# Kernel tuning notes

Hardware: AMD Instinct MI355X
Metric: run time of the kernel (lower is better)

## Reference

```python
import jax, jax.numpy as jnp
import numpy as np

N_NODES = 10000
N_EDGES = 160000
HID = 256
NBOND = 6
NATOM = 62
NLAYERS = 6


def _lin_init(key, fan_in, fan_out):
    # torch nn.Linear default: U(-1/sqrt(fan_in), 1/sqrt(fan_in))
    kw, kb = jax.random.split(key)
    bound = 1.0 / np.sqrt(fan_in)
    w = jax.random.uniform(kw, (fan_in, fan_out), jnp.float32, -bound, bound)
    b = jax.random.uniform(kb, (fan_out,), jnp.float32, -bound, bound)
    return w, b


def setup_inputs() -> dict:
    key = jax.random.key(0)
    ks = jax.random.split(key, 32)
    atom_features = jax.random.normal(ks[0], (N_NODES, NATOM), jnp.float32)
    edge_index = jax.random.randint(ks[1], (2, N_EDGES), 0, N_NODES, jnp.int64 if jax.config.jax_enable_x64 else jnp.int32)
    edge_features = jax.random.normal(ks[2], (N_EDGES, NBOND), jnp.float32)

    embed_w, embed_b = _lin_init(ks[3], NATOM, HID)

    msg_in = 2 * HID + NBOND  # 518
    mw1, mb1, mw2, mb2 = [], [], [], []
    uw1, ub1, uw2, ub2 = [], [], [], []
    for i in range(NLAYERS):
        k = jax.random.split(ks[4 + i], 4)
        w, b = _lin_init(k[0], msg_in, HID); mw1.append(w); mb1.append(b)
        w, b = _lin_init(k[1], HID, HID); mw2.append(w); mb2.append(b)
        w, b = _lin_init(k[2], 2 * HID, HID); uw1.append(w); ub1.append(b)
        w, b = _lin_init(k[3], HID, HID); uw2.append(w); ub2.append(b)

    r_w1, r_b1 = _lin_init(ks[20], HID, HID)
    r_w2, r_b2 = _lin_init(ks[21], HID, HID // 2)
    r_w3, r_b3 = _lin_init(ks[22], HID // 2, 1)

    return {
        "atom_features": atom_features,
        "edge_index": edge_index,
        "edge_features": edge_features,
        "embed_w": embed_w, "embed_b": embed_b,
        "msg_w1": jnp.stack(mw1), "msg_b1": jnp.stack(mb1),
        "msg_w2": jnp.stack(mw2), "msg_b2": jnp.stack(mb2),
        "upd_w1": jnp.stack(uw1), "upd_b1": jnp.stack(ub1),
        "upd_w2": jnp.stack(uw2), "upd_b2": jnp.stack(ub2),
        "r_w1": r_w1, "r_b1": r_b1,
        "r_w2": r_w2, "r_b2": r_b2,
        "r_w3": r_w3, "r_b3": r_b3,
    }


def _mlp2(x, w1, b1, w2, b2):
    return jnp.maximum(x @ w1 + b1, 0.0) @ w2 + b2


def reference(atom_features, edge_index, edge_features,
              embed_w, embed_b,
              msg_w1, msg_b1, msg_w2, msg_b2,
              upd_w1, upd_b1, upd_w2, upd_b2,
              r_w1, r_b1, r_w2, r_b2, r_w3, r_b3):
    src, dst = edge_index[0], edge_index[1]
    n = atom_features.shape[0]
    x = atom_features @ embed_w + embed_b  # [N, H]
    for l in range(msg_w1.shape[0]):
        # per-edge gather + concat -> message MLP
        msg_in = jnp.concatenate([x[src], x[dst], edge_features], axis=-1)  # [E, 2H+B]
        msgs = _mlp2(msg_in, msg_w1[l], msg_b1[l], msg_w2[l], msg_b2[l])  # [E, H]
        # scatter-add into dst nodes
        agg = jax.ops.segment_sum(msgs, dst, num_segments=n)  # [N, H]
        x = _mlp2(jnp.concatenate([x, agg], axis=-1), upd_w1[l], upd_b1[l], upd_w2[l], upd_b2[l])
    # readout (dropout is identity in eval mode)
    h = jnp.maximum(x @ r_w1 + r_b1, 0.0)
    h = jnp.maximum(h @ r_w2 + r_b2, 0.0)
    out = h @ r_w3 + r_b3  # [N, 1]
    return out.mean(axis=0)  # [1]
```

## Files before the change

kernel.cpp:

```cpp
#include <hip/hip_runtime.h>
#include <hip/hip_bf16.h>
#include <hip/hip_fp16.h>


#define HID 256

typedef _Float16 h8 __attribute__((ext_vector_type(8)));
typedef float f32x4 __attribute__((ext_vector_type(4)));

__device__ __forceinline__ void unpack_h8(const int4& r, float* f) {
    const __half2* h = reinterpret_cast<const __half2*>(&r);
#pragma unroll
    for (int k = 0; k < 4; ++k) {
        float2 t = __half22float2(h[k]);
        f[2 * k] = t.x;
        f[2 * k + 1] = t.y;
    }
}

__device__ __forceinline__ void unpack_h4(const int2& r, float* f) {
    const __half2* h = reinterpret_cast<const __half2*>(&r);
    float2 t0 = __half22float2(h[0]);
    float2 t1 = __half22float2(h[1]);
    f[0] = t0.x; f[1] = t0.y; f[2] = t1.x; f[3] = t1.y;
}

__device__ __forceinline__ void gld16(const void* g, void* l) {
    __builtin_amdgcn_global_load_lds(
        (const __attribute__((address_space(1))) void*)g,
        (__attribute__((address_space(3))) void*)l, 16, 0, 0);
}

__device__ __forceinline__ int swz(int row) { return (row + (row >> 2)) & 3; }


__global__ void hist_act_kernel(const int* __restrict__ dst, int* __restrict__ deg,
                                int E, const float* __restrict__ atom,
                                __half* __restrict__ atomH, int NA) {
    int i = blockIdx.x * blockDim.x + threadIdx.x;
    if (i < E) atomicAdd(&deg[dst[i]], 1);
    if (i < NA) {
        int r = i >> 3, seg = i & 7;
        h8 v;
#pragma unroll
        for (int j = 0; j < 8; ++j) {
            int c = seg * 8 + j;
            v[j] = (_Float16)((c < 62) ? atom[(size_t)r * 62 + c] : 0.f);
        }
        *reinterpret_cast<h8*>(&atomH[(size_t)r * 64 + seg * 8]) = v;
    }
}

__global__ __launch_bounds__(256) void scan_kernel(
    const int* __restrict__ deg, int* __restrict__ offs, float* __restrict__ degf, int n) {
    __shared__ int ws[4];
    const int t = threadIdx.x;
    const int lane = t & 63;
    const int w = t >> 6;
    const int per = (n + 255) / 256;
    const int s = t * per;
    const int e = min(s + per, n);
    int sum = 0;
    for (int i = s; i < e; ++i) sum += deg[i];
    int v = sum;
#pragma unroll
    for (int off = 1; off < 64; off <<= 1) {
        int u = __shfl_up(v, off, 64);
        if (lane >= off) v += u;
    }
    if (lane == 63) ws[w] = v;
    __syncthreads();
    if (t == 0) {
        int c = 0;
#pragma unroll
        for (int i = 0; i < 4; ++i) { int x = ws[i]; ws[i] = c; c += x; }
    }
    __syncthreads();
    int run = ws[w] + v - sum;
    for (int i = s; i < e; ++i) {
        int d = deg[i];
        offs[i] = run;
        degf[i] = (float)d;
        run += d;
    }
    if (e == n) offs[n] = run;
}


struct CDesc {
    const float* src;
    __half* dst;
    int Kreal, Kpad, srcN, tile0, dstStride;
};
struct CTab {
    CDesc d[32];
    int nd;
};

__device__ void convert_body(const CTab& tab, int bid) {
    int idx = 0;
    for (int i = 1; i < tab.nd; ++i)
        if (tab.d[i].tile0 <= bid) idx = i;
    const CDesc d = tab.d[idx];
    const int q = bid - d.tile0;
    const int ntN = d.srcN >> 6;
    const int kb = (q / ntN) * 32;
    const int nb = (q % ntN) * 64;
    const int n = nb + (threadIdx.x & 63);
    const int k0 = kb + (threadIdx.x >> 6) * 8;
    h8 v;
#pragma unroll
    for (int j = 0; j < 8; ++j) {
        int k = k0 + j;
        v[j] = (_Float16)((k < d.Kreal) ? d.src[(size_t)k * d.srcN + n] : 0.f);
    }
    *reinterpret_cast<h8*>(&d.dst[(size_t)n * d.dstStride + k0]) = v;
}

__global__ __launch_bounds__(256) void scatter_conv_kernel(
    const int* __restrict__ src, const int* __restrict__ dst,
    const int* __restrict__ offs, int* __restrict__ cursor,
    int* __restrict__ csr_src, const float* __restrict__ ef,
    __half* __restrict__ ef8, int E, int sblocks, CTab tab) {
    if ((int)blockIdx.x < sblocks) {
        int i = blockIdx.x * blockDim.x + threadIdx.x;
        if (i < E) {
            int d = dst[i];
            int pos = atomicAdd(&cursor[d], 1);
            int idx = offs[d] + pos;
            csr_src[idx] = src[i];
            const float* s6 = ef + (size_t)i * 6;
            unsigned short h[8];
#pragma unroll
            for (int j = 0; j < 6; ++j) h[j] = __half_as_ushort(__float2half_rn(s6[j]));
            h[6] = 0; h[7] = 0;
            int4 pk;
            pk.x = (int)(h[0] | ((unsigned)h[1] << 16));
            pk.y = (int)(h[2] | ((unsigned)h[3] << 16));
            pk.z = (int)(h[4] | ((unsigned)h[5] << 16));
            pk.w = (int)(h[6] | ((unsigned)h[7] << 16));
            *reinterpret_cast<int4*>(ef8 + (size_t)idx * 8) = pk;
        }
    } else {
        convert_body(tab, blockIdx.x - sblocks);
    }
}


struct BDesc { float* out; const float* base; const float* v1; const float* B1;
               const float* v2; const float* B2; };
struct BTab { BDesc d[31]; };


#define ASTR 40

struct FDesc { const float* U2; const __half* Wfb; __half* dst; int stride; };
struct FTab { FDesc d[22]; };

__device__ void fold_tile(unsigned char* ldsraw, const FDesc& dd, int t4) {
    _Float16* Ah = (_Float16*)ldsraw;
    _Float16* Bh = (_Float16*)(ldsraw + 64 * ASTR * 2);
    const int rowBase = (t4 >> 2) * 64;
    const int colBase = (t4 & 3) * 64;

    const int tid = threadIdx.x;
    const int lane = tid & 63;
    const int wave = tid >> 6;
    const int waveM = (wave >> 1) * 32;
    const int waveN = (wave & 1) * 32;
    const int m0 = lane & 15;
    const int quad = lane >> 4;
    const int sr = tid >> 2;
    const int sseg = tid & 3;

    const f32x4 z = {0.f, 0.f, 0.f, 0.f};
    f32x4 acc[2][2] = {{z, z}, {z, z}};

    for (int kb = 0; kb < 256; kb += 32) {
        {
            size_t off = (size_t)(rowBase + sr) * 256 + kb + sseg * 8;
            *reinterpret_cast<int4*>(&Ah[sr * ASTR + sseg * 8]) =
                *reinterpret_cast<const int4*>(&dd.Wfb[off]);
        }
        {
            const float* Bp = dd.U2 + (size_t)(colBase + sr) * 256 + kb + sseg * 8;
            float4 u0 = *reinterpret_cast<const float4*>(Bp);
            float4 u1 = *reinterpret_cast<const float4*>(Bp + 4);
            h8 v;
            v[0] = (_Float16)u0.x; v[1] = (_Float16)u0.y;
            v[2] = (_Float16)u0.z; v[3] = (_Float16)u0.w;
            v[4] = (_Float16)u1.x; v[5] = (_Float16)u1.y;
            v[6] = (_Float16)u1.z; v[7] = (_Float16)u1.w;
            *reinterpret_cast<h8*>(&Bh[sr * ASTR + sseg * 8]) = v;
        }
        __syncthreads();

        const h8 a0 = *reinterpret_cast<const h8*>(&Ah[(waveM + m0) * ASTR + quad * 8]);
        const h8 a1 = *reinterpret_cast<const h8*>(&Ah[(waveM + 16 + m0) * ASTR + quad * 8]);
        const h8 b0 = *reinterpret_cast<const h8*>(&Bh[(waveN + m0) * ASTR + quad * 8]);
        const h8 b1 = *reinterpret_cast<const h8*>(&Bh[(waveN + 16 + m0) * ASTR + quad * 8]);

        acc[0][0] = __builtin_amdgcn_mfma_f32_16x16x32_f16(a0, b0, acc[0][0], 0, 0, 0);
        acc[0][1] = __builtin_amdgcn_mfma_f32_16x16x32_f16(a0, b1, acc[0][1], 0, 0, 0);
        acc[1][0] = __builtin_amdgcn_mfma_f32_16x16x32_f16(a1, b0, acc[1][0], 0, 0, 0);
        acc[1][1] = __builtin_amdgcn_mfma_f32_16x16x32_f16(a1, b1, acc[1][1], 0, 0, 0);

        __syncthreads();
    }

#pragma unroll
    for (int tm = 0; tm < 2; ++tm)
#pragma unroll
        for (int reg = 0; reg < 4; ++reg) {
            int n = rowBase + waveM + tm * 16 + quad * 4 + reg;
#pragma unroll
            for (int tn = 0; tn < 2; ++tn) {
                int k = colBase + waveN + tn * 16 + m0;
                dd.dst[(size_t)n * dd.stride + k] = __float2half_rn(acc[tm][tn][reg]);
            }
        }
}


template <int TN>
__device__ void gemm_tile(
    unsigned char* lds, int bx, int by,
    const __half* __restrict__ A, int lda, const __half* __restrict__ A2,
    const __half* __restrict__ W, int K,
    const float* __restrict__ bias, const float* __restrict__ bias2,
    const float* __restrict__ rowscale,
    __half* __restrict__ C, int M, int Nc, int do_relu) {
    constexpr int BUF = 4096 + TN * 2048;

    const int tid = threadIdx.x;
    const int lane = tid & 63;
    const int wave = tid >> 6;
    const int m0 = lane & 15;
    const int quad = lane >> 4;
    const int waveM = (wave >> 1) * 32;
    const int waveN = (wave & 1) * (TN * 16);
    const int rowBase = bx * 64;
    const int colBase = by * (TN * 32);

    const int sa_r = tid >> 2;
    const int sa_ks = (tid & 3) ^ swz(sa_r);
    const int sa_row = min(rowBase + sa_r, M - 1);
    const int sb_r1 = sa_r + 64;
    const int sb_ks1 = (tid & 3) ^ swz(sb_r1);

    int aoff[2], boff[TN];
#pragma unroll
    for (int tm = 0; tm < 2; ++tm) {
        int r = waveM + tm * 16 + m0;
        aoff[tm] = ((r << 2) + (quad ^ swz(r))) << 4;
    }
#pragma unroll
    for (int tn = 0; tn < TN; ++tn) {
        int r = waveN + tn * 16 + m0;
        boff[tn] = 4096 + (((r << 2) + (quad ^ swz(r))) << 4);
    }

    const f32x4 z = {0.f, 0.f, 0.f, 0.f};
    f32x4 acc[2][TN];
#pragma unroll
    for (int tm = 0; tm < 2; ++tm)
#pragma unroll
        for (int tn = 0; tn < TN; ++tn) acc[tm][tn] = z;

    const __half* ga = A + (size_t)sa_row * lda + sa_ks * 8;
    const __half* ga2 = A2 ? A2 + (size_t)sa_row * lda + sa_ks * 8 : nullptr;
    const __half* gb0 = W + (size_t)(colBase + sa_r) * K + sa_ks * 8;
    const __half* gb1 = W + (size_t)(colBase + sb_r1) * K + sb_ks1 * 8;

    auto issue = [&](int p, int kb) {
        unsigned char* base = lds + p * BUF;
        const __half* as = (A2 && kb >= 256) ? (ga2 + (kb - 256)) : (ga + kb);
        gld16(as, base + wave * 1024);
        gld16(gb0 + kb, base + 4096 + wave * 1024);
        if constexpr (TN == 4) gld16(gb1 + kb, base + 8192 + wave * 1024);
    };

    issue(0, 0);
    int p = 0;
    for (int kb = 0; kb < K; kb += 32) {
        const bool has_next = (kb + 32 < K);
        if (has_next) issue(p ^ 1, kb + 32);
        if (has_next) {
            if constexpr (TN == 4)
                asm volatile("s_waitcnt vmcnt(3)" ::: "memory");
            else
                asm volatile("s_waitcnt vmcnt(2)" ::: "memory");
        } else {
            asm volatile("s_waitcnt vmcnt(0)" ::: "memory");
        }
        asm volatile("s_barrier" ::: "memory");

        const unsigned char* base = lds + p * BUF;
        h8 ah[2], bh[TN];
#pragma unroll
        for (int tm = 0; tm < 2; ++tm)
            ah[tm] = *reinterpret_cast<const h8*>(base + aoff[tm]);
#pragma unroll
        for (int tn = 0; tn < TN; ++tn)
            bh[tn] = *reinterpret_cast<const h8*>(base + boff[tn]);
#pragma unroll
        for (int tm = 0; tm < 2; ++tm)
#pragma unroll
            for (int tn = 0; tn < TN; ++tn)
                acc[tm][tn] = __builtin_amdgcn_mfma_f32_16x16x32_f16(
                    ah[tm], bh[tn], acc[tm][tn], 0, 0, 0);
        asm volatile("s_waitcnt lgkmcnt(0)" ::: "memory");
        asm volatile("s_barrier" ::: "memory");
        p ^= 1;
    }

    float cb[TN], db[TN];
    int col[TN];
#pragma unroll
    for (int tn = 0; tn < TN; ++tn) {
        col[tn] = colBase + waveN + tn * 16 + m0;
        cb[tn] = bias ? bias[col[tn]] : 0.f;
        db[tn] = bias2 ? bias2[col[tn]] : 0.f;
    }
#pragma unroll
    for (int tm = 0; tm < 2; ++tm) {
#pragma unroll
        for (int reg = 0; reg < 4; ++reg) {
            int row = rowBase + waveM + tm * 16 + quad * 4 + reg;
            if (row >= M) continue;
            float rs = rowscale ? rowscale[row] : 0.0f;
#pragma unroll
            for (int tn = 0; tn < TN; ++tn) {
                float v = acc[tm][tn][reg] + cb[tn] + rs * db[tn];
                if (do_relu) v = fmaxf(v, 0.f);
                C[(size_t)row * Nc + col[tn]] = __float2half_rn(v);
            }
        }
    }
}

template <int TN>
__global__ __launch_bounds__(256) void mfma_gemm(
    const __half* __restrict__ A, int lda, const __half* __restrict__ A2,
    const __half* __restrict__ W, int K,
    const float* __restrict__ bias, const float* __restrict__ bias2,
    const float* __restrict__ rowscale,
    __half* __restrict__ C, int M, int Nc, int do_relu) {
    __shared__ __align__(16) unsigned char lds[2 * (4096 + TN * 2048)];
    gemm_tile<TN>(lds, blockIdx.x, blockIdx.y, A, lda, A2, W, K,
                  bias, bias2, rowscale, C, M, Nc, do_relu);
}


__global__ __launch_bounds__(256) void fold_bias_embed_kernel(
    FTab ft, BTab bt, int fblocks, int bblocks,
    const __half* __restrict__ atomH, const __half* __restrict__ w_emb,
    const float* __restrict__ emb_b, __half* __restrict__ outX,
    int M, int mblk) {
    __shared__ __align__(16) unsigned char lds[16384];
    int b = blockIdx.x;
    if (b < fblocks) {
        fold_tile(lds, ft.d[b >> 4], b & 15);
        return;
    }
    b -= fblocks;
    if (b < bblocks) {
        const BDesc d = bt.d[b];
        const int j = threadIdx.x;
        float acc = d.base ? d.base[j] : 0.f;
        if (d.v1)
            for (int k = 0; k < 256; ++k) acc = fmaf(d.v1[k], d.B1[(size_t)k * 256 + j], acc);
        if (d.v2)
            for (int k = 0; k < 256; ++k) acc = fmaf(d.v2[k], d.B2[(size_t)k * 256 + j], acc);
        d.out[j] = acc;
        return;
    }
    b -= bblocks;
    gemm_tile<2>(lds, b % mblk, b / mblk, atomH, 64, nullptr, w_emb, 64,
                 emb_b, nullptr, nullptr, outX, M, HID, 0);
}


__global__ __launch_bounds__(256) void aggregate_kernel(
    const __half* __restrict__ PQ, const __half* __restrict__ ef8,
    const int* __restrict__ offs, const int* __restrict__ csr_src,
    const float* __restrict__ W1c, __half* __restrict__ Hagg, int n) {
    const int wave = threadIdx.x >> 6;
    const int lane = threadIdx.x & 63;
    const int node = blockIdx.x * 4 + wave;
    if (node >= n) return;
    const int ch = lane * 4;

    float wc[6][4];
#pragma unroll
    for (int k = 0; k < 6; ++k) {
        float4 w0 = *reinterpret_cast<const float4*>(W1c + k * HID + ch);
        wc[k][0] = w0.x; wc[k][1] = w0.y; wc[k][2] = w0.z; wc[k][3] = w0.w;
    }
    float qb[4];
    unpack_h4(*reinterpret_cast<const int2*>(PQ + (size_t)node * 512 + 256 + ch), qb);

    float acc[4] = {0.f, 0.f, 0.f, 0.f};

    auto fma_edge = [&](const int2& praw, const int4& eraw) {
        float p[4], e[8];
        unpack_h4(praw, p);
        unpack_h8(eraw, e);
#pragma unroll
        for (int i = 0; i < 4; ++i) {
            float h = p[i] + qb[i];
            h = fmaf(e[0], wc[0][i], h);
            h = fmaf(e[1], wc[1][i], h);
            h = fmaf(e[2], wc[2][i], h);
            h = fmaf(e[3], wc[3][i], h);
            h = fmaf(e[4], wc[4][i], h);
            h = fmaf(e[5], wc[5][i], h);
            acc[i] += fmaxf(h, 0.f);
        }
    };

    const int beg = offs[node];
    const int end = offs[node + 1];
    int j = beg;

    while (j + 6 <= end) {
        int s0 = csr_src[j];
        int s1 = csr_src[j + 1];
        int s2 = csr_src[j + 2];
        int s3 = csr_src[j + 3];
        int s4 = csr_src[j + 4];
        int s5 = csr_src[j + 5];
        int4 e0 = *reinterpret_cast<const int4*>(ef8 + (size_t)j * 8);
        int4 e1 = *reinterpret_cast<const int4*>(ef8 + (size_t)(j + 1) * 8);
        int4 e2 = *reinterpret_cast<const int4*>(ef8 + (size_t)(j + 2) * 8);
        int4 e3 = *reinterpret_cast<const int4*>(ef8 + (size_t)(j + 3) * 8);
        int4 e4 = *reinterpret_cast<const int4*>(ef8 + (size_t)(j + 4) * 8);
        int4 e5 = *reinterpret_cast<const int4*>(ef8 + (size_t)(j + 5) * 8);
        int2 p0 = *reinterpret_cast<const int2*>(PQ + (size_t)s0 * 512 + ch);
        int2 p1 = *reinterpret_cast<const int2*>(PQ + (size_t)s1 * 512 + ch);
        int2 p2 = *reinterpret_cast<const int2*>(PQ + (size_t)s2 * 512 + ch);
        int2 p3 = *reinterpret_cast<const int2*>(PQ + (size_t)s3 * 512 + ch);
        int2 p4 = *reinterpret_cast<const int2*>(PQ + (size_t)s4 * 512 + ch);
        int2 p5 = *reinterpret_cast<const int2*>(PQ + (size_t)s5 * 512 + ch);
        fma_edge(p0, e0);
        fma_edge(p1, e1);
        fma_edge(p2, e2);
        fma_edge(p3, e3);
        fma_edge(p4, e4);
        fma_edge(p5, e5);
        j += 6;
    }
    while (j + 2 <= end) {
        int s0 = csr_src[j];
        int s1 = csr_src[j + 1];
        int4 e0 = *reinterpret_cast<const int4*>(ef8 + (size_t)j * 8);
        int4 e1 = *reinterpret_cast<const int4*>(ef8 + (size_t)(j + 1) * 8);
        int2 p0 = *reinterpret_cast<const int2*>(PQ + (size_t)s0 * 512 + ch);
        int2 p1 = *reinterpret_cast<const int2*>(PQ + (size_t)s1 * 512 + ch);
        fma_edge(p0, e0);
        fma_edge(p1, e1);
        j += 2;
    }
    if (j < end) {
        int s = csr_src[j];
        int4 e = *reinterpret_cast<const int4*>(ef8 + (size_t)j * 8);
        int2 pw = *reinterpret_cast<const int2*>(PQ + (size_t)s * 512 + ch);
        fma_edge(pw, e);
    }

    unsigned short hs[4];
#pragma unroll
    for (int i = 0; i < 4; ++i) hs[i] = __half_as_ushort(__float2half_rn(acc[i]));
    int2 pk;
    pk.x = (int)(hs[0] | ((unsigned)hs[1] << 16));
    pk.y = (int)(hs[2] | ((unsigned)hs[3] << 16));
    *reinterpret_cast<int2*>(Hagg + (size_t)node * HID + ch) = pk;
}


__global__ __launch_bounds__(256) void readout_kernel(
    const __half* __restrict__ U5, const __half* __restrict__ wF,
    const float* __restrict__ cbF, const __half* __restrict__ wR2,
    const float* __restrict__ bR2, const float* __restrict__ w3,
    const float* __restrict__ b3, float* __restrict__ accum,
    int* __restrict__ done, float* __restrict__ outp, int M, int nblocks) {
    __shared__ __align__(16) unsigned char lds[24576 + 64 * 272 * 2];
    _Float16* h1 = (_Float16*)(lds + 24576);

    const int tid = threadIdx.x;
    const int lane = tid & 63;
    const int wave = tid >> 6;
    const int m0 = lane & 15;
    const int quad = lane >> 4;
    const int waveM = (wave >> 1) * 32;
    const int waveN = (wave & 1) * 64;
    const int rowBase = blockIdx.x * 64;

    const int sa_r = tid >> 2;
    const int sa_ks = (tid & 3) ^ swz(sa_r);
    const int sa_row = min(rowBase + sa_r, M - 1);
    const int sb_r1 = sa_r + 64;
    const int sb_ks1 = (tid & 3) ^ swz(sb_r1);

    int aoff[2], boff[4];
#pragma unroll
    for (int tm = 0; tm < 2; ++tm) {
        int r = waveM + tm * 16 + m0;
        aoff[tm] = ((r << 2) + (quad ^ swz(r))) << 4;
    }
#pragma unroll
    for (int tn = 0; tn < 4; ++tn) {
        int r = waveN + tn * 16 + m0;
        boff[tn] = (((r << 2) + (quad ^ swz(r))) << 4);
    }

    constexpr int BUF = 4096 + 4 * 2048;
    const f32x4 z = {0.f, 0.f, 0.f, 0.f};

    for (int half = 0; half < 2; ++half) {
        const __half* W = wF + (size_t)(half * 128) * 256;
        f32x4 acc[2][4] = {{z, z, z, z}, {z, z, z, z}};
        const __half* ga = U5 + (size_t)sa_row * 256 + sa_ks * 8;
        const __half* gb0 = W + (size_t)sa_r * 256 + sa_ks * 8;
        const __half* gb1 = W + (size_t)sb_r1 * 256 + sb_ks1 * 8;

        auto issue = [&](int p, int kb) {
            unsigned char* base = lds + p * BUF;
            gld16(ga + kb, base + wave * 1024);
            gld16(gb0 + kb, base + 4096 + wave * 1024);
            gld16(gb1 + kb, base + 8192 + wave * 1024);
        };
        issue(0, 0);
        int p = 0;
        for (int kb = 0; kb < 256; kb += 32) {
            const bool has_next = (kb + 32 < 256);
            if (has_next) issue(p ^ 1, kb + 32);
            if (has_next) asm volatile("s_waitcnt vmcnt(3)" ::: "memory");
            else asm volatile("s_waitcnt vmcnt(0)" ::: "memory");
            asm volatile("s_barrier" ::: "memory");
            const unsigned char* base = lds + p * BUF;
            h8 ah[2], bh[4];
#pragma unroll
            for (int tm = 0; tm < 2; ++tm)
                ah[tm] = *reinterpret_cast<const h8*>(base + aoff[tm]);
#pragma unroll
            for (int tn = 0; tn < 4; ++tn)
                bh[tn] = *reinterpret_cast<const h8*>(base + 4096 + boff[tn]);
#pragma unroll
            for (int tm = 0; tm < 2; ++tm)
#pragma unroll
                for (int tn = 0; tn < 4; ++tn)
                    acc[tm][tn] = __builtin_amdgcn_mfma_f32_16x16x32_f16(
                        ah[tm], bh[tn], acc[tm][tn], 0, 0, 0);
            asm volatile("s_waitcnt lgkmcnt(0)" ::: "memory");
            asm volatile("s_barrier" ::: "memory");
            p ^= 1;
        }
#pragma unroll
        for (int tm = 0; tm < 2; ++tm)
#pragma unroll
            for (int reg = 0; reg < 4; ++reg) {
                int r = waveM + tm * 16 + quad * 4 + reg;
#pragma unroll
                for (int tn = 0; tn < 4; ++tn) {
                    int c = half * 128 + waveN + tn * 16 + m0;
                    float v = acc[tm][tn][reg] + cbF[c];
                    h1[r * 272 + c] = (_Float16)fmaxf(v, 0.f);
                }
            }
        __syncthreads();
    }

    f32x4 acc2[2][4] = {{z, z, z, z}, {z, z, z, z}};
    auto issueB = [&](int p, int kb) {
        unsigned char* base = lds + p * 8192;
        gld16(wR2 + (size_t)sa_r * 256 + sa_ks * 8 + kb, base + wave * 1024);
        gld16(wR2 + (size_t)sb_r1 * 256 + sb_ks1 * 8 + kb, base + 4096 + wave * 1024);
    };
    issueB(0, 0);
    int p = 0;
    for (int kb = 0; kb < 256; kb += 32) {
        const bool has_next = (kb + 32 < 256);
        if (has_next) issueB(p ^ 1, kb + 32);
        if (has_next) asm volatile("s_waitcnt vmcnt(2)" ::: "memory");
        else asm volatile("s_waitcnt vmcnt(0)" ::: "memory");
        asm volatile("s_barrier" ::: "memory");
        const unsigned char* base = lds + p * 8192;
        h8 ah[2], bh[4];
#pragma unroll
        for (int tm = 0; tm < 2; ++tm)
            ah[tm] = *reinterpret_cast<const h8*>(
                &h1[(waveM + tm * 16 + m0) * 272 + kb + quad * 8]);
#pragma unroll
        for (int tn = 0; tn < 4; ++tn)
            bh[tn] = *reinterpret_cast<const h8*>(base + boff[tn]);
#pragma unroll
        for (int tm = 0; tm < 2; ++tm)
#pragma unroll
            for (int tn = 0; tn < 4; ++tn)
                acc2[tm][tn] = __builtin_amdgcn_mfma_f32_16x16x32_f16(
                    ah[tm], bh[tn], acc2[tm][tn], 0, 0, 0);
        asm volatile("s_waitcnt lgkmcnt(0)" ::: "memory");
        asm volatile("s_barrier" ::: "memory");
        p ^= 1;
    }

    float s = 0.f;
#pragma unroll
    for (int tm = 0; tm < 2; ++tm)
#pragma unroll
        for (int reg = 0; reg < 4; ++reg) {
            int row = rowBase + waveM + tm * 16 + quad * 4 + reg;
            if (row >= M) continue;
#pragma unroll
            for (int tn = 0; tn < 4; ++tn) {
                int c = waveN + tn * 16 + m0;
                float v = acc2[tm][tn][reg] + bR2[c];
                s += fmaxf(v, 0.f) * w3[c];
            }
        }
    __syncthreads();
    float* red = (float*)lds;
    red[tid] = s;
    __syncthreads();
    for (int off = 128; off > 0; off >>= 1) {
        if (tid < off) red[tid] += red[tid + off];
        __syncthreads();
    }
    if (tid == 0) {
        atomicAdd(accum, red[0]);
        __threadfence();
        int old = atomicAdd(done, 1);
        if (old == nblocks - 1) {
            float tot = atomicAdd(accum, 0.0f);
            outp[0] = tot / (float)M + b3[0];
        }
    }
}


extern "C" void kernel_launch(void* const* d_in, const int* in_sizes, int n_in,
                              void* d_out, int out_size, void* d_ws, size_t ws_size,
                              hipStream_t stream) {
    const float* atom   = (const float*)d_in[0];
    const int*   eidx   = (const int*)d_in[1];
    const float* ef     = (const float*)d_in[2];
    const float* emb_w  = (const float*)d_in[3];
    const float* emb_b  = (const float*)d_in[4];
    const float* msg_w1 = (const float*)d_in[5];
    const float* msg_b1 = (const float*)d_in[6];
    const float* msg_w2 = (const float*)d_in[7];
    const float* msg_b2 = (const float*)d_in[8];
    const float* upd_w1 = (const float*)d_in[9];
    const float* upd_b1 = (const float*)d_in[10];
    const float* upd_w2 = (const float*)d_in[11];
    const float* upd_b2 = (const float*)d_in[12];
    const float* r_w1   = (const float*)d_in[13];
    const float* r_b1   = (const float*)d_in[14];
    const float* r_w2   = (const float*)d_in[15];
    const float* r_b2   = (const float*)d_in[16];
    const float* r_w3   = (const float*)d_in[17];
    const float* r_b3   = (const float*)d_in[18];

    const int N = in_sizes[0] / 62;
    const int E = in_sizes[1] / 2;
    const int L = in_sizes[5] / (518 * 256);
    const int* src = eidx;
    const int* dst = eidx + E;

    char* wp = (char*)d_ws;
    auto alloc = [&](size_t bytes) -> void* {
        void* p = (void*)wp;
        wp += (bytes + 255) & ~(size_t)255;
        return p;
    };
    int*   deg     = (int*)alloc((size_t)N * 4);
    int*   cursor  = (int*)alloc((size_t)N * 4);
    float* accum   = (float*)alloc(256);
    int*   done    = (int*)((char*)accum + 16);
    size_t zero_bytes = (size_t)((char*)accum - (char*)d_ws) + 256;
    float* degf    = (float*)alloc((size_t)N * 4);
    int*   offs    = (int*)alloc((size_t)(N + 1) * 4);
    int*   csr_src = (int*)alloc((size_t)E * 4);
    __half* ef8    = (__half*)alloc((size_t)E * 8 * 2);

    const int SQ_P = 256 * 256;
    __half* w_emb = (__half*)alloc((size_t)256 * 64 * 2);
    __half* w_r2  = (__half*)alloc((size_t)128 * 256 * 2);
    __half* wF    = (__half*)alloc((size_t)SQ_P * 2);
    __half *wPQ[6], *wUPD[6];
    for (int l = 0; l < L; ++l) {
        wPQ[l]  = (__half*)alloc((size_t)512 * 256 * 2);
        wUPD[l] = (__half*)alloc((size_t)256 * 512 * 2);
    }
    __half* fb[22];
    for (int i = 0; i < 22; ++i) fb[i] = (__half*)alloc((size_t)SQ_P * 2);
    float* bvec = (float*)alloc((size_t)19 * 256 * 4);
    float* b512 = (float*)alloc((size_t)L * 512 * 4);

    __half* atomH = (__half*)alloc((size_t)N * 64 * 2);
    __half* bufX0 = (__half*)alloc((size_t)N * HID * 2);
    __half* bufX1 = (__half*)alloc((size_t)N * HID * 2);
    __half* PQ    = (__half*)alloc((size_t)N * 512 * 2);
    __half* HaggH = (__half*)alloc((size_t)N * HID * 2);

    hipMemsetAsync(d_ws, 0, zero_bytes, stream);

    const int hag = max(E, N * 8);
    hist_act_kernel<<<(hag + 255) / 256, 256, 0, stream>>>(dst, deg, E, atom, atomH, N * 8);
    scan_kernel<<<1, 256, 0, stream>>>(deg, offs, degf, N);

    CTab ct1;
    int nd = 0, tiles = 0;
    auto addDesc = [&](const float* s, __half* dh, int Kreal, int Kpad, int srcN,
                       int dstStride) {
        ct1.d[nd] = {s, dh, Kreal, Kpad, srcN, tiles, dstStride};
        tiles += (Kpad / 32) * (srcN / 64);
        ++nd;
    };
    addDesc(emb_w, w_emb, 62, 64, 256, 64);
    addDesc(msg_w1, wPQ[0], 256, 256, 256, 256);
    addDesc(msg_w1 + 256 * 256, wPQ[0] + SQ_P, 256, 256, 256, 256);
    addDesc(upd_w1, wUPD[0] + 256, 256, 256, 256, 512);
    addDesc(r_w2, w_r2, 256, 256, 128, 256);
    for (int l = 1; l < L; ++l) {
        addDesc(msg_w1 + (size_t)l * 518 * 256,             fb[l - 1], 256, 256, 256, 256);
        addDesc(msg_w1 + (size_t)l * 518 * 256 + 256 * 256, fb[4 + l], 256, 256, 256, 256);
        addDesc(upd_w1 + (size_t)l * 512 * 256,             fb[9 + l], 256, 256, 256, 256);
    }
    for (int l = 0; l < L; ++l)
        addDesc(upd_w1 + (size_t)l * 512 * 256 + 256 * 256, fb[15 + l], 256, 256, 256, 256);
    addDesc(r_w1, fb[21], 256, 256, 256, 256);
    ct1.nd = nd;

    const int sblocks = (E + 255) / 256;
    scatter_conv_kernel<<<sblocks + tiles, 256, 0, stream>>>(
        src, dst, offs, cursor, csr_src, ef, ef8, E, sblocks, ct1);

    FTab ft;
    for (int l = 1; l < L; ++l) {
        const float* U2p = upd_w2 + (size_t)(l - 1) * SQ_P;
        ft.d[l - 1] = {U2p, fb[l - 1], wPQ[l], 256};
        ft.d[4 + l] = {U2p, fb[4 + l], wPQ[l] + SQ_P, 256};
        ft.d[9 + l] = {U2p, fb[9 + l], wUPD[l] + 256, 512};
    }
    for (int l = 0; l < L; ++l)
        ft.d[15 + l] = {msg_w2 + (size_t)l * SQ_P, fb[15 + l], wUPD[l], 512};
    ft.d[21] = {upd_w2 + (size_t)5 * SQ_P, fb[21], wF, 256};

    BTab bt;
    int nb = 0;
    for (int l = 0; l < L; ++l) {
        const float* ub2p = (l > 0) ? upd_b2 + (size_t)(l - 1) * 256 : nullptr;
        bt.d[nb++] = {b512 + (size_t)l * 512 + 256, msg_b1 + (size_t)l * 256,
                      ub2p, msg_w1 + (size_t)l * 518 * 256,
                      ub2p, msg_w1 + (size_t)l * 518 * 256 + 256 * 256};
        bt.d[nb++] = {b512 + (size_t)l * 512, nullptr, nullptr, nullptr, nullptr, nullptr};
        bt.d[nb++] = {bvec + (size_t)(6 + l) * 256, upd_b1 + (size_t)l * 256,
                      ub2p, upd_w1 + (size_t)l * 512 * 256, nullptr, nullptr};
        bt.d[nb++] = {bvec + (size_t)(12 + l) * 256, nullptr,
                      msg_b2 + (size_t)l * 256, upd_w1 + (size_t)l * 512 * 256 + 256 * 256,
                      nullptr, nullptr};
    }
    bt.d[nb++] = {bvec + (size_t)18 * 256, r_b1, upd_b2 + (size_t)5 * 256, r_w1,
                  nullptr, nullptr};

    const int mblk = (N + 63) / 64;
    const int fblocks = 22 * 16;
    fold_bias_embed_kernel<<<fblocks + nb + mblk * 4, 256, 0, stream>>>(
        ft, bt, fblocks, nb, atomH, w_emb, emb_b, bufX0, N, mblk);

    dim3 blk(256);
    __half* U_prev = bufX0;
    __half* U_next = bufX1;
    for (int l = 0; l < L; ++l) {
        const float* w1c = msg_w1 + (size_t)l * 518 * 256 + 512 * 256;

        mfma_gemm<4><<<dim3(mblk, 4), blk, 0, stream>>>(
            U_prev, HID, nullptr, wPQ[l], HID,
            b512 + (size_t)l * 512, nullptr, nullptr,
            PQ, N, 512, 0);
        aggregate_kernel<<<(N + 3) / 4, blk, 0, stream>>>(
            PQ, ef8, offs, csr_src, w1c, HaggH, N);
        mfma_gemm<2><<<dim3(mblk, 4), blk, 0, stream>>>(
            HaggH, HID, U_prev, wUPD[l], 512,
            bvec + (size_t)(6 + l) * 256, bvec + (size_t)(12 + l) * 256, degf,
            U_next, N, HID, 1);
        __half* t = U_prev; U_prev = U_next; U_next = t;
    }

    readout_kernel<<<mblk, blk, 0, stream>>>(
        U_prev, wF, bvec + (size_t)18 * 256, w_r2, r_b2, r_w3, r_b3,
        accum, done, (float*)d_out, N, mblk);
}
```

Before: 446.6 us.

## Fuse aggregation, update GEMM and next-layer projection into one per-layer kernel

Result: slower. 592.0 us (+32.5%).

```diff
diff --git a/kernel.cpp b/kernel.cpp
--- a/kernel.cpp
+++ b/kernel.cpp
@@ -225,10 +225,9 @@
 template <int TN>
 __device__ void gemm_tile(
     unsigned char* lds, int bx, int by,
-    const __half* __restrict__ A, int lda, const __half* __restrict__ A2,
+    const __half* __restrict__ A, int lda,
     const __half* __restrict__ W, int K,
-    const float* __restrict__ bias, const float* __restrict__ bias2,
-    const float* __restrict__ rowscale,
+    const float* __restrict__ bias,
     __half* __restrict__ C, int M, int Nc, int do_relu) {
     constexpr int BUF = 4096 + TN * 2048;
 
@@ -268,14 +267,12 @@
         for (int tn = 0; tn < TN; ++tn) acc[tm][tn] = z;
 
     const __half* ga = A + (size_t)sa_row * lda + sa_ks * 8;
-    const __half* ga2 = A2 ? A2 + (size_t)sa_row * lda + sa_ks * 8 : nullptr;
     const __half* gb0 = W + (size_t)(colBase + sa_r) * K + sa_ks * 8;
     const __half* gb1 = W + (size_t)(colBase + sb_r1) * K + sb_ks1 * 8;
 
     auto issue = [&](int p, int kb) {
         unsigned char* base = lds + p * BUF;
-        const __half* as = (A2 && kb >= 256) ? (ga2 + (kb - 256)) : (ga + kb);
-        gld16(as, base + wave * 1024);
+        gld16(ga + kb, base + wave * 1024);
         gld16(gb0 + kb, base + 4096 + wave * 1024);
         if constexpr (TN == 4) gld16(gb1 + kb, base + 8192 + wave * 1024);
     };
@@ -314,13 +311,12 @@
         p ^= 1;
     }
 
-    float cb[TN], db[TN];
+    float cb[TN];
     int col[TN];
 #pragma unroll
     for (int tn = 0; tn < TN; ++tn) {
         col[tn] = colBase + waveN + tn * 16 + m0;
         cb[tn] = bias ? bias[col[tn]] : 0.f;
-        db[tn] = bias2 ? bias2[col[tn]] : 0.f;
     }
 #pragma unroll
     for (int tm = 0; tm < 2; ++tm) {
@@ -328,10 +324,9 @@
         for (int reg = 0; reg < 4; ++reg) {
             int row = rowBase + waveM + tm * 16 + quad * 4 + reg;
             if (row >= M) continue;
-            float rs = rowscale ? rowscale[row] : 0.0f;
 #pragma unroll
             for (int tn = 0; tn < TN; ++tn) {
-                float v = acc[tm][tn][reg] + cb[tn] + rs * db[tn];
+                float v = acc[tm][tn][reg] + cb[tn];
                 if (do_relu) v = fmaxf(v, 0.f);
                 C[(size_t)row * Nc + col[tn]] = __float2half_rn(v);
             }
@@ -341,14 +336,12 @@
 
 template <int TN>
 __global__ __launch_bounds__(256) void mfma_gemm(
-    const __half* __restrict__ A, int lda, const __half* __restrict__ A2,
+    const __half* __restrict__ A, int lda,
     const __half* __restrict__ W, int K,
-    const float* __restrict__ bias, const float* __restrict__ bias2,
-    const float* __restrict__ rowscale,
+    const float* __restrict__ bias,
     __half* __restrict__ C, int M, int Nc, int do_relu) {
     __shared__ __align__(16) unsigned char lds[2 * (4096 + TN * 2048)];
-    gemm_tile<TN>(lds, blockIdx.x, blockIdx.y, A, lda, A2, W, K,
-                  bias, bias2, rowscale, C, M, Nc, do_relu);
+    gemm_tile<TN>(lds, blockIdx.x, blockIdx.y, A, lda, W, K, bias, C, M, Nc, do_relu);
 }
 
 
@@ -376,105 +369,259 @@
         return;
     }
     b -= bblocks;
-    gemm_tile<2>(lds, b % mblk, b / mblk, atomH, 64, nullptr, w_emb, 64,
-                 emb_b, nullptr, nullptr, outX, M, HID, 0);
-}
-
-
-__global__ __launch_bounds__(256) void aggregate_kernel(
-    const __half* __restrict__ PQ, const __half* __restrict__ ef8,
+    gemm_tile<2>(lds, b % mblk, b / mblk, atomH, 64, w_emb, 64,
+                 emb_b, outX, M, HID, 0);
+}
+
+
+__global__ __launch_bounds__(512, 1) void layer_kernel(
+    const __half* __restrict__ PQRin, const __half* __restrict__ ef8,
     const int* __restrict__ offs, const int* __restrict__ csr_src,
-    const float* __restrict__ W1c, __half* __restrict__ Hagg, int n) {
-    const int wave = threadIdx.x >> 6;
-    const int lane = threadIdx.x & 63;
-    const int node = blockIdx.x * 4 + wave;
-    if (node >= n) return;
-    const int ch = lane * 4;
-
-    float wc[6][4];
-#pragma unroll
-    for (int k = 0; k < 6; ++k) {
-        float4 w0 = *reinterpret_cast<const float4*>(W1c + k * HID + ch);
-        wc[k][0] = w0.x; wc[k][1] = w0.y; wc[k][2] = w0.z; wc[k][3] = w0.w;
-    }
-    float qb[4];
-    unpack_h4(*reinterpret_cast<const int2*>(PQ + (size_t)node * 512 + 256 + ch), qb);
-
-    float acc[4] = {0.f, 0.f, 0.f, 0.f};
-
-    auto fma_edge = [&](const int2& praw, const int4& eraw) {
-        float p[4], e[8];
-        unpack_h4(praw, p);
-        unpack_h8(eraw, e);
-#pragma unroll
-        for (int i = 0; i < 4; ++i) {
-            float h = p[i] + qb[i];
-            h = fmaf(e[0], wc[0][i], h);
-            h = fmaf(e[1], wc[1][i], h);
-            h = fmaf(e[2], wc[2][i], h);
-            h = fmaf(e[3], wc[3][i], h);
-            h = fmaf(e[4], wc[4][i], h);
-            h = fmaf(e[5], wc[5][i], h);
-            acc[i] += fmaxf(h, 0.f);
-        }
+    const float* __restrict__ W1c,
+    const __half* __restrict__ wM3,
+    const float* __restrict__ bias, const float* __restrict__ bias2,
+    const float* __restrict__ degf,
+    const __half* __restrict__ wPQRnext, const float* __restrict__ b768next,
+    __half* __restrict__ PQRout, __half* __restrict__ Ufinal, int M) {
+    __shared__ __align__(16) unsigned char lds[16384 + 64 * 272 * 2];
+    _Float16* TAH = (_Float16*)(lds + 16384);
+
+    const int tid = threadIdx.x;
+    const int w = tid >> 6;
+    const int lane = tid & 63;
+    const int rowBase = (int)blockIdx.x * 64;
+
+    {
+        const int ch = lane * 4;
+        float wc[6][4];
+#pragma unroll
+        for (int k = 0; k < 6; ++k) {
+            float4 w0 = *reinterpret_cast<const float4*>(W1c + k * HID + ch);
+            wc[k][0] = w0.x; wc[k][1] = w0.y; wc[k][2] = w0.z; wc[k][3] = w0.w;
+        }
+        for (int i = 0; i < 8; ++i) {
+            const int ln = w * 8 + i;
+            const int node = rowBase + ln;
+            float acc4[4] = {0.f, 0.f, 0.f, 0.f};
+            if (node < M) {
+                float qb[4];
+                unpack_h4(*reinterpret_cast<const int2*>(
+                              PQRin + (size_t)node * 768 + 256 + ch), qb);
+                auto fma_edge = [&](const int2& praw, const int4& eraw) {
+                    float p[4], e[8];
+                    unpack_h4(praw, p);
+                    unpack_h8(eraw, e);
+#pragma unroll
+                    for (int c = 0; c < 4; ++c) {
+                        float h = p[c] + qb[c];
+                        h = fmaf(e[0], wc[0][c], h);
+                        h = fmaf(e[1], wc[1][c], h);
+                        h = fmaf(e[2], wc[2][c], h);
+                        h = fmaf(e[3], wc[3][c], h);
+                        h = fmaf(e[4], wc[4][c], h);
+                        h = fmaf(e[5], wc[5][c], h);
+                        acc4[c] += fmaxf(h, 0.f);
+                    }
+                };
+                const int beg = offs[node];
+                const int end = offs[node + 1];
+                int j = beg;
+                while (j + 6 <= end) {
+                    int s0 = csr_src[j];
+                    int s1 = csr_src[j + 1];
+                    int s2 = csr_src[j + 2];
+                    int s3 = csr_src[j + 3];
+                    int s4 = csr_src[j + 4];
+                    int s5 = csr_src[j + 5];
+                    int4 e0 = *reinterpret_cast<const int4*>(ef8 + (size_t)j * 8);
+                    int4 e1 = *reinterpret_cast<const int4*>(ef8 + (size_t)(j + 1) * 8);
+                    int4 e2 = *reinterpret_cast<const int4*>(ef8 + (size_t)(j + 2) * 8);
+                    int4 e3 = *reinterpret_cast<const int4*>(ef8 + (size_t)(j + 3) * 8);
+                    int4 e4 = *reinterpret_cast<const int4*>(ef8 + (size_t)(j + 4) * 8);
+                    int4 e5 = *reinterpret_cast<const int4*>(ef8 + (size_t)(j + 5) * 8);
+                    int2 p0 = *reinterpret_cast<const int2*>(PQRin + (size_t)s0 * 768 + ch);
+                    int2 p1 = *reinterpret_cast<const int2*>(PQRin + (size_t)s1 * 768 + ch);
+                    int2 p2 = *reinterpret_cast<const int2*>(PQRin + (size_t)s2 * 768 + ch);
+                    int2 p3 = *reinterpret_cast<const int2*>(PQRin + (size_t)s3 * 768 + ch);
+                    int2 p4 = *reinterpret_cast<const int2*>(PQRin + (size_t)s4 * 768 + ch);
+                    int2 p5 = *reinterpret_cast<const int2*>(PQRin + (size_t)s5 * 768 + ch);
+                    fma_edge(p0, e0);
+                    fma_edge(p1, e1);
+                    fma_edge(p2, e2);
+                    fma_edge(p3, e3);
+                    fma_edge(p4, e4);
+                    fma_edge(p5, e5);
+                    j += 6;
+                }
+                while (j + 2 <= end) {
+                    int s0 = csr_src[j];
+                    int s1 = csr_src[j + 1];
+                    int4 e0 = *reinterpret_cast<const int4*>(ef8 + (size_t)j * 8);
+                    int4 e1 = *reinterpret_cast<const int4*>(ef8 + (size_t)(j + 1) * 8);
+                    int2 p0 = *reinterpret_cast<const int2*>(PQRin + (size_t)s0 * 768 + ch);
+                    int2 p1 = *reinterpret_cast<const int2*>(PQRin + (size_t)s1 * 768 + ch);
+                    fma_edge(p0, e0);
+                    fma_edge(p1, e1);
+                    j += 2;
+                }
+                if (j < end) {
+                    int s = csr_src[j];
+                    int4 e = *reinterpret_cast<const int4*>(ef8 + (size_t)j * 8);
+                    int2 pw = *reinterpret_cast<const int2*>(PQRin + (size_t)s * 768 + ch);
+                    fma_edge(pw, e);
+                }
+            }
+            unsigned short hs[4];
+#pragma unroll
+            for (int c = 0; c < 4; ++c)
+                hs[c] = __half_as_ushort(__float2half_rn(acc4[c]));
+            int2 pk;
+            pk.x = (int)(hs[0] | ((unsigned)hs[1] << 16));
+            pk.y = (int)(hs[2] | ((unsigned)hs[3] << 16));
+            *reinterpret_cast<int2*>(&TAH[ln * 272 + ch]) = pk;
+        }
+    }
+    __syncthreads();
+
+    const int m0 = lane & 15;
+    const int quad = lane >> 4;
+    const int wM = (w >> 2) * 32;
+    const int wN = (w & 3) * 32;
+    const f32x4 z = {0.f, 0.f, 0.f, 0.f};
+
+    auto issueW = [&](const __half* Wp, int colOfs, int p, int kb) {
+        const int r0 = tid >> 2;
+        const int s0 = (tid & 3) ^ swz(r0);
+        gld16(Wp + (size_t)(colOfs + r0) * 256 + kb + s0 * 8,
+              lds + p * 8192 + w * 1024);
     };
 
-    const int beg = offs[node];
-    const int end = offs[node + 1];
-    int j = beg;
-
-    while (j + 6 <= end) {
-        int s0 = csr_src[j];
-        int s1 = csr_src[j + 1];
-        int s2 = csr_src[j + 2];
-        int s3 = csr_src[j + 3];
-        int s4 = csr_src[j + 4];
-        int s5 = csr_src[j + 5];
-        int4 e0 = *reinterpret_cast<const int4*>(ef8 + (size_t)j * 8);
-        int4 e1 = *reinterpret_cast<const int4*>(ef8 + (size_t)(j + 1) * 8);
-        int4 e2 = *reinterpret_cast<const int4*>(ef8 + (size_t)(j + 2) * 8);
-        int4 e3 = *reinterpret_cast<const int4*>(ef8 + (size_t)(j + 3) * 8);
-        int4 e4 = *reinterpret_cast<const int4*>(ef8 + (size_t)(j + 4) * 8);
-        int4 e5 = *reinterpret_cast<const int4*>(ef8 + (size_t)(j + 5) * 8);
-        int2 p0 = *reinterpret_cast<const int2*>(PQ + (size_t)s0 * 512 + ch);
-        int2 p1 = *reinterpret_cast<const int2*>(PQ + (size_t)s1 * 512 + ch);
-        int2 p2 = *reinterpret_cast<const int2*>(PQ + (size_t)s2 * 512 + ch);
-        int2 p3 = *reinterpret_cast<const int2*>(PQ + (size_t)s3 * 512 + ch);
-        int2 p4 = *reinterpret_cast<const int2*>(PQ + (size_t)s4 * 512 + ch);
-        int2 p5 = *reinterpret_cast<const int2*>(PQ + (size_t)s5 * 512 + ch);
-        fma_edge(p0, e0);
-        fma_edge(p1, e1);
-        fma_edge(p2, e2);
-        fma_edge(p3, e3);
-        fma_edge(p4, e4);
-        fma_edge(p5, e5);
-        j += 6;
-    }
-    while (j + 2 <= end) {
-        int s0 = csr_src[j];
-        int s1 = csr_src[j + 1];
-        int4 e0 = *reinterpret_cast<const int4*>(ef8 + (size_t)j * 8);
-        int4 e1 = *reinterpret_cast<const int4*>(ef8 + (size_t)(j + 1) * 8);
-        int2 p0 = *reinterpret_cast<const int2*>(PQ + (size_t)s0 * 512 + ch);
-        int2 p1 = *reinterpret_cast<const int2*>(PQ + (size_t)s1 * 512 + ch);
-        fma_edge(p0, e0);
-        fma_edge(p1, e1);
-        j += 2;
-    }
-    if (j < end) {
-        int s = csr_src[j];
-        int4 e = *reinterpret_cast<const int4*>(ef8 + (size_t)j * 8);
-        int2 pw = *reinterpret_cast<const int2*>(PQ + (size_t)s * 512 + ch);
-        fma_edge(pw, e);
-    }
-
-    unsigned short hs[4];
-#pragma unroll
-    for (int i = 0; i < 4; ++i) hs[i] = __half_as_ushort(__float2half_rn(acc[i]));
-    int2 pk;
-    pk.x = (int)(hs[0] | ((unsigned)hs[1] << 16));
-    pk.y = (int)(hs[2] | ((unsigned)hs[3] << 16));
-    *reinterpret_cast<int2*>(Hagg + (size_t)node * HID + ch) = pk;
+    f32x4 accB[2][2][2];
+#pragma unroll
+    for (int ps = 0; ps < 2; ++ps)
+#pragma unroll
+        for (int tm = 0; tm < 2; ++tm)
+#pragma unroll
+            for (int tn = 0; tn < 2; ++tn) accB[ps][tm][tn] = z;
+
+    for (int ps = 0; ps < 2; ++ps) {
+        const int colBase = ps * 128;
+        issueW(wM3, colBase, 0, 0);
+        int p = 0;
+        for (int kb = 0; kb < 256; kb += 32) {
+            const bool hn = kb + 32 < 256;
+            if (hn) issueW(wM3, colBase, p ^ 1, kb + 32);
+            if (hn) asm volatile("s_waitcnt vmcnt(1)" ::: "memory");
+            else    asm volatile("s_waitcnt vmcnt(0)" ::: "memory");
+            asm volatile("s_barrier" ::: "memory");
+            const unsigned char* bb = lds + p * 8192;
+            h8 ah[2], bh[2];
+#pragma unroll
+            for (int tm = 0; tm < 2; ++tm)
+                ah[tm] = *reinterpret_cast<const h8*>(
+                    &TAH[(wM + tm * 16 + m0) * 272 + kb + quad * 8]);
+#pragma unroll
+            for (int tn = 0; tn < 2; ++tn) {
+                int r = wN + tn * 16 + m0;
+                bh[tn] = *reinterpret_cast<const h8*>(
+                    bb + (((r << 2) + (quad ^ swz(r))) << 4));
+            }
+#pragma unroll
+            for (int tm = 0; tm < 2; ++tm)
+#pragma unroll
+                for (int tn = 0; tn < 2; ++tn)
+                    accB[ps][tm][tn] = __builtin_amdgcn_mfma_f32_16x16x32_f16(
+                        ah[tm], bh[tn], accB[ps][tm][tn], 0, 0, 0);
+            asm volatile("s_waitcnt lgkmcnt(0)" ::: "memory");
+            asm volatile("s_barrier" ::: "memory");
+            p ^= 1;
+        }
+    }
+#pragma unroll
+    for (int ps = 0; ps < 2; ++ps) {
+        float cb[2], db[2];
+        int colp[2];
+#pragma unroll
+        for (int tn = 0; tn < 2; ++tn) {
+            colp[tn] = ps * 128 + wN + tn * 16 + m0;
+            cb[tn] = bias[colp[tn]];
+            db[tn] = bias2[colp[tn]];
+        }
+#pragma unroll
+        for (int tm = 0; tm < 2; ++tm)
+#pragma unroll
+            for (int reg = 0; reg < 4; ++reg) {
+                const int lrow = wM + tm * 16 + quad * 4 + reg;
+                const int row = rowBase + lrow;
+                const float rs = degf[min(row, M - 1)];
+#pragma unroll
+                for (int tn = 0; tn < 2; ++tn) {
+                    float v = accB[ps][tm][tn][reg] + cb[tn] + rs * db[tn];
+                    if (row < M)
+                        v += __half2float(PQRin[(size_t)row * 768 + 512 + colp[tn]]);
+                    v = fmaxf(v, 0.f);
+                    TAH[lrow * 272 + colp[tn]] = (_Float16)v;
+                    if (Ufinal && row < M)
+                        Ufinal[(size_t)row * 256 + colp[tn]] = __float2half_rn(v);
+                }
+            }
+    }
+    __syncthreads();
+
+    if (wPQRnext) {
+        for (int ps = 0; ps < 6; ++ps) {
+            const int colBase = ps * 128;
+            f32x4 acc2[2][2] = {{z, z}, {z, z}};
+            issueW(wPQRnext, colBase, 0, 0);
+            int p = 0;
+            for (int kb = 0; kb < 256; kb += 32) {
+                const bool hn = kb + 32 < 256;
+                if (hn) issueW(wPQRnext, colBase, p ^ 1, kb + 32);
+                if (hn) asm volatile("s_waitcnt vmcnt(1)" ::: "memory");
+                else    asm volatile("s_waitcnt vmcnt(0)" ::: "memory");
+                asm volatile("s_barrier" ::: "memory");
+                const unsigned char* bb = lds + p * 8192;
+                h8 ah[2], bh[2];
+#pragma unroll
+                for (int tm = 0; tm < 2; ++tm)
+                    ah[tm] = *reinterpret_cast<const h8*>(
+                        &TAH[(wM + tm * 16 + m0) * 272 + kb + quad * 8]);
+#pragma unroll
+                for (int tn = 0; tn < 2; ++tn) {
+                    int r = wN + tn * 16 + m0;
+                    bh[tn] = *reinterpret_cast<const h8*>(
+                        bb + (((r << 2) + (quad ^ swz(r))) << 4));
+                }
+#pragma unroll
+                for (int tm = 0; tm < 2; ++tm)
+#pragma unroll
+                    for (int tn = 0; tn < 2; ++tn)
+                        acc2[tm][tn] = __builtin_amdgcn_mfma_f32_16x16x32_f16(
+                            ah[tm], bh[tn], acc2[tm][tn], 0, 0, 0);
+                asm volatile("s_waitcnt lgkmcnt(0)" ::: "memory");
+                asm volatile("s_barrier" ::: "memory");
+                p ^= 1;
+            }
+            float cbn[2];
+            int coln[2];
+#pragma unroll
+            for (int tn = 0; tn < 2; ++tn) {
+                coln[tn] = colBase + wN + tn * 16 + m0;
+                cbn[tn] = b768next[coln[tn]];
+            }
+#pragma unroll
+            for (int tm = 0; tm < 2; ++tm)
+#pragma unroll
+                for (int reg = 0; reg < 4; ++reg) {
+                    const int row = rowBase + wM + tm * 16 + quad * 4 + reg;
+                    if (row >= M) continue;
+#pragma unroll
+                    for (int tn = 0; tn < 2; ++tn)
+                        PQRout[(size_t)row * 768 + coln[tn]] =
+                            __float2half_rn(acc2[tm][tn][reg] + cbn[tn]);
+                }
+        }
+    }
 }
 
 
@@ -688,21 +835,21 @@
     __half* w_emb = (__half*)alloc((size_t)256 * 64 * 2);
     __half* w_r2  = (__half*)alloc((size_t)128 * 256 * 2);
     __half* wF    = (__half*)alloc((size_t)SQ_P * 2);
-    __half *wPQ[6], *wUPD[6];
+    __half *wPQR[6], *wM3_[6];
     for (int l = 0; l < L; ++l) {
-        wPQ[l]  = (__half*)alloc((size_t)512 * 256 * 2);
-        wUPD[l] = (__half*)alloc((size_t)256 * 512 * 2);
+        wPQR[l] = (__half*)alloc((size_t)768 * 256 * 2);
+        wM3_[l] = (__half*)alloc((size_t)SQ_P * 2);
     }
     __half* fb[22];
     for (int i = 0; i < 22; ++i) fb[i] = (__half*)alloc((size_t)SQ_P * 2);
     float* bvec = (float*)alloc((size_t)19 * 256 * 4);
-    float* b512 = (float*)alloc((size_t)L * 512 * 4);
+    float* b768 = (float*)alloc((size_t)L * 768 * 4);
 
     __half* atomH = (__half*)alloc((size_t)N * 64 * 2);
     __half* bufX0 = (__half*)alloc((size_t)N * HID * 2);
     __half* bufX1 = (__half*)alloc((size_t)N * HID * 2);
-    __half* PQ    = (__half*)alloc((size_t)N * 512 * 2);
-    __half* HaggH = (__half*)alloc((size_t)N * HID * 2);
+    __half* PQR_A = (__half*)alloc((size_t)N * 768 * 2);
+    __half* PQR_B = (__half*)alloc((size_t)N * 768 * 2);
 
     hipMemsetAsync(d_ws, 0, zero_bytes, stream);
 
@@ -719,9 +866,9 @@
         ++nd;
     };
     addDesc(emb_w, w_emb, 62, 64, 256, 64);
-    addDesc(msg_w1, wPQ[0], 256, 256, 256, 256);
-    addDesc(msg_w1 + 256 * 256, wPQ[0] + SQ_P, 256, 256, 256, 256);
-    addDesc(upd_w1, wUPD[0] + 256, 256, 256, 256, 512);
+    addDesc(msg_w1, wPQR[0], 256, 256, 256, 256);
+    addDesc(msg_w1 + 256 * 256, wPQR[0] + SQ_P, 256, 256, 256, 256);
+    addDesc(upd_w1, wPQR[0] + 2 * SQ_P, 256, 256, 256, 256);
     addDesc(r_w2, w_r2, 256, 256, 128, 256);
     for (int l = 1; l < L; ++l) {
         addDesc(msg_w1 + (size_t)l * 518 * 256,             fb[l - 1], 256, 256, 256, 256);
@@ -740,22 +887,23 @@
     FTab ft;
     for (int l = 1; l < L; ++l) {
         const float* U2p = upd_w2 + (size_t)(l - 1) * SQ_P;
-        ft.d[l - 1] = {U2p, fb[l - 1], wPQ[l], 256};
-        ft.d[4 + l] = {U2p, fb[4 + l], wPQ[l] + SQ_P, 256};
-        ft.d[9 + l] = {U2p, fb[9 + l], wUPD[l] + 256, 512};
+        ft.d[l - 1] = {U2p, fb[l - 1], wPQR[l], 256};
+        ft.d[4 + l] = {U2p, fb[4 + l], wPQR[l] + SQ_P, 256};
+        ft.d[9 + l] = {U2p, fb[9 + l], wPQR[l] + 2 * SQ_P, 256};
     }
     for (int l = 0; l < L; ++l)
-        ft.d[15 + l] = {msg_w2 + (size_t)l * SQ_P, fb[15 + l], wUPD[l], 512};
+        ft.d[15 + l] = {msg_w2 + (size_t)l * SQ_P, fb[15 + l], wM3_[l], 256};
     ft.d[21] = {upd_w2 + (size_t)5 * SQ_P, fb[21], wF, 256};
 
     BTab bt;
     int nb = 0;
     for (int l = 0; l < L; ++l) {
         const float* ub2p = (l > 0) ? upd_b2 + (size_t)(l - 1) * 256 : nullptr;
-        bt.d[nb++] = {b512 + (size_t)l * 512 + 256, msg_b1 + (size_t)l * 256,
+        bt.d[nb++] = {b768 + (size_t)l * 768 + 256, msg_b1 + (size_t)l * 256,
                       ub2p, msg_w1 + (size_t)l * 518 * 256,
                       ub2p, msg_w1 + (size_t)l * 518 * 256 + 256 * 256};
-        bt.d[nb++] = {b512 + (size_t)l * 512, nullptr, nullptr, nullptr, nullptr, nullptr};
+        bt.d[nb++] = {b768 + (size_t)l * 768, nullptr, nullptr, nullptr, nullptr, nullptr};
+        bt.d[nb++] = {b768 + (size_t)l * 768 + 512, nullptr, nullptr, nullptr, nullptr, nullptr};
         bt.d[nb++] = {bvec + (size_t)(6 + l) * 256, upd_b1 + (size_t)l * 256,
                       ub2p, upd_w1 + (size_t)l * 512 * 256, nullptr, nullptr};
         bt.d[nb++] = {bvec + (size_t)(12 + l) * 256, nullptr,
@@ -770,26 +918,24 @@
     fold_bias_embed_kernel<<<fblocks + nb + mblk * 4, 256, 0, stream>>>(
         ft, bt, fblocks, nb, atomH, w_emb, emb_b, bufX0, N, mblk);
 
-    dim3 blk(256);
-    __half* U_prev = bufX0;
-    __half* U_next = bufX1;
+    mfma_gemm<4><<<dim3(mblk, 6), 256, 0, stream>>>(
+        bufX0, 256, wPQR[0], 256, b768, PQR_A, N, 768, 0);
+
+    __half* Pin = PQR_A;
+    __half* Pout = PQR_B;
     for (int l = 0; l < L; ++l) {
+        const bool last = (l == L - 1);
         const float* w1c = msg_w1 + (size_t)l * 518 * 256 + 512 * 256;
-
-        mfma_gemm<4><<<dim3(mblk, 4), blk, 0, stream>>>(
-            U_prev, HID, nullptr, wPQ[l], HID,
-            b512 + (size_t)l * 512, nullptr, nullptr,
-            PQ, N, 512, 0);
-        aggregate_kernel<<<(N + 3) / 4, blk, 0, stream>>>(
-            PQ, ef8, offs, csr_src, w1c, HaggH, N);
-        mfma_gemm<2><<<dim3(mblk, 4), blk, 0, stream>>>(
-            HaggH, HID, U_prev, wUPD[l], 512,
+        layer_kernel<<<mblk, 512, 0, stream>>>(
+            Pin, ef8, offs, csr_src, w1c, wM3_[l],
             bvec + (size_t)(6 + l) * 256, bvec + (size_t)(12 + l) * 256, degf,
-            U_next, N, HID, 1);
-        __half* t = U_prev; U_prev = U_next; U_next = t;
-    }
-
-    readout_kernel<<<mblk, blk, 0, stream>>>(
-        U_prev, wF, bvec + (size_t)18 * 256, w_r2, r_b2, r_w3, r_b3,
+            last ? nullptr : wPQR[l + 1],
+            last ? nullptr : (b768 + (size_t)(l + 1) * 768),
+            Pout, last ? bufX1 : nullptr, N);
+        __half* t = Pin; Pin = Pout; Pout = t;
+    }
+
+    readout_kernel<<<mblk, 256, 0, stream>>>(
+        bufX1, wF, bvec + (size_t)18 * 256, w_r2, r_b2, r_w3, r_b3,
         accum, done, (float*)d_out, N, mblk);
 }
```
